# Optimization experiments

Measured on AMD Instinct MI355X. Metric: run time of the kernel, lower is better.

The kernel has to match this reference:

```python
import jax, jax.numpy as jnp
import numpy as np

B, L, LQ = 64, 4096, 128
D = 32        # input_dim (value channels)
ET = 128      # embed_time
NH = 1        # num_heads
H = 128       # nhidden
NC = 6        # n_classes


def _time_emb(tt, lin_w, lin_b, per_w, per_b):
    # tt [..., T] -> [..., T, ET]; cat(Linear(1,1)(t), sin(Linear(1,ET-1)(t)))
    tt = tt[..., None]
    out1 = tt * lin_w[0, 0] + lin_b
    out2 = jnp.sin(tt @ per_w + per_b)
    return jnp.concatenate([out1, out2], axis=-1)


def _gru_dir(xs, wih, whh, bih, bhh, reverse):
    # xs [B, T, I] -> [B, T, H]; torch GRU gate math
    xs_t = jnp.swapaxes(xs, 0, 1)              # [T, B, I]
    if reverse:
        xs_t = xs_t[::-1]
    gi_all = xs_t @ wih.T + bih                # [T, B, 3H] precomputed input gates
    h0 = jnp.zeros((xs.shape[0], H), xs.dtype)

    def step(h, gi):
        gh = h @ whh.T + bhh
        ir, iz, inn = jnp.split(gi, 3, axis=-1)
        hr, hz, hn = jnp.split(gh, 3, axis=-1)
        r = jax.nn.sigmoid(ir + hr)
        z = jax.nn.sigmoid(iz + hz)
        n = jnp.tanh(inn + r * hn)
        h_new = (1.0 - z) * n + z * h
        return h_new, h_new

    _, ys = jax.lax.scan(step, h0, gi_all)     # [T, B, H]
    if reverse:
        ys = ys[::-1]
    return jnp.swapaxes(ys, 0, 1)


def _bigru(xs, wih, whh, bih, bhh):
    fwd = _gru_dir(xs, wih[0], whh[0], bih[0], bhh[0], False)
    bwd = _gru_dir(xs, wih[1], whh[1], bih[1], bhh[1], True)
    return jnp.concatenate([fwd, bwd], axis=-1)


def setup_inputs() -> dict:
    ks = jax.random.split(jax.random.key(0), 32)
    w = lambda i, s: jax.random.normal(ks[i], s, jnp.float32) * 0.05
    G3 = 3 * H
    return {
        "x": jax.random.normal(ks[0], (B, L, D), jnp.float32),
        "time_steps": jax.random.uniform(ks[1], (B, L), dtype=jnp.float32),
        "query_times": jnp.linspace(0.0, 1.0, LQ, dtype=jnp.float32),
        "lin_w": w(2, (1, 1)), "lin_b": w(3, (1,)),
        "per_w": w(4, (1, ET - 1)), "per_b": w(5, (ET - 1,)),
        "wq": w(6, (ET, ET)), "bq": w(7, (ET,)),
        "wk": w(8, (ET, ET)), "bk": w(9, (ET,)),
        "wo": w(10, (NH * D, H)), "bo": w(11, (H,)),
        "gru0_wih": w(12, (2, G3, H)), "gru0_whh": w(13, (2, G3, H)),
        "gru0_bih": w(14, (2, G3)), "gru0_bhh": w(15, (2, G3)),
        "gru1_wih": w(16, (2, G3, 2 * H)), "gru1_whh": w(17, (2, G3, H)),
        "gru1_bih": w(18, (2, G3)), "gru1_bhh": w(19, (2, G3)),
        "c1_w": w(20, (2 * H, 128)), "c1_b": w(21, (128,)),
        "c2_w": w(22, (128, 64)), "c2_b": w(23, (64,)),
        "c3_w": w(24, (64, NC)), "c3_b": w(25, (NC,)),
    }


def reference(x, time_steps, query_times, lin_w, lin_b, per_w, per_b,
              wq, bq, wk, bk, wo, bo,
              gru0_wih, gru0_whh, gru0_bih, gru0_bhh,
              gru1_wih, gru1_whh, gru1_bih, gru1_bhh,
              c1_w, c1_b, c2_w, c2_b, c3_w, c3_b):
    ek = ET // NH
    # learned time embeddings
    q = _time_emb(query_times[None, :], lin_w, lin_b, per_w, per_b)  # [1, LQ, ET]
    k = _time_emb(time_steps, lin_w, lin_b, per_w, per_b)            # [B, L, ET]
    # per-head projections
    qp = (q @ wq + bq).reshape(1, LQ, NH, ek).transpose(0, 2, 1, 3)[0]  # [NH, LQ, ek]
    kp = (k @ wk + bk).reshape(B, L, NH, ek).transpose(0, 2, 1, 3)      # [B, NH, L, ek]
    # mTAN attention: scores are channel-independent (mask=None), so the
    # per-channel repeat+softmax reduces to a single softmax over keys.
    scores = jnp.einsum('hqe,bhke->bhqk', qp, kp) / jnp.sqrt(jnp.float32(ek))
    p = jax.nn.softmax(scores, axis=-1)                                 # [B, NH, LQ, L]
    att = jnp.einsum('bhqk,bkd->bqhd', p, x).reshape(B, LQ, NH * D)
    att_out = att @ wo + bo                                             # [B, LQ, H]
    # 2-layer bidirectional GRU
    g0 = _bigru(att_out, gru0_wih, gru0_whh, gru0_bih, gru0_bhh)        # [B, LQ, 2H]
    g1 = _bigru(g0, gru1_wih, gru1_whh, gru1_bih, gru1_bhh)             # [B, LQ, 2H]
    class_in = jnp.concatenate([g1[:, -1, :H], g1[:, 0, H:]], axis=1)   # [B, 2H]
    out = ((class_in @ c1_w + c1_b) @ c2_w + c2_b) @ c3_w + c3_b        # [B, NC]
    return out
```

## Files before the change

kernel.cpp:

```cpp
#include <hip/hip_runtime.h>
#include <math.h>

#define Bn   64
#define Ln   4096
#define LQn  128
#define Dn   32
#define ETn  128
#define Hn   128
#define G3n  384
#define NDEG 12

typedef __attribute__((ext_vector_type(2))) float f32x2;

#define DPPF(x, ctrl) __int_as_float(__builtin_amdgcn_update_dpp(0, __float_as_int(x), (ctrl), 0xF, 0xF, true))
#define QP_XOR1 0xB1
#define QP_XOR2 0x4E
#define QP_B0   0x00
#define QP_B1   0x55
#define QP_B2   0xAA
#define QP_B3   0xFF

__device__ __forceinline__ float sin_poly(float x) {
    const float x2 = x * x;
    float r = -1.9841270114e-04f;
    r = fmaf(r, x2,  8.3333337680e-03f);
    r = fmaf(r, x2, -1.6666667163e-01f);
    return fmaf(r * x2, x, x);
}
__device__ __forceinline__ float cos_poly(float x) {
    const float x2 = x * x;
    float r =  2.4801587642e-05f;
    r = fmaf(r, x2, -1.3888888899e-03f);
    r = fmaf(r, x2,  4.1666667908e-02f);
    r = fmaf(r, x2, -5.0000000000e-01f);
    return fmaf(r, x2, 1.0f);
}

#define WS_C    0
#define WS_WT   4096
#define WS_B2   (WS_WT + 768*32)
#define WS_CLS  (WS_B2 + 1024)
#define WS_G0   (WS_CLS + Bn*2*Hn)
#define WS_GI   (WS_G0 + Bn*LQn*2*Hn)
#define WS_QPB  WS_G0
#define WS_BAS  (WS_G0 + 16384)
#define WS_ACCP WS_G0
#define WS_SP   (WS_G0 + 1048576)

__global__ __launch_bounds__(128) void k_basis(
    const float* __restrict__ per_w, const float* __restrict__ per_b,
    float* __restrict__ basis)
{
    const int j = threadIdx.x;
    if (j >= ETn - 1) return;
    const float w = per_w[j], b = per_b[j];
    const float sb = sin_poly(b), cb = cos_poly(b);
    float wp = 1.f;
#pragma unroll
    for (int d = 0; d < NDEG; ++d) {
        const float sd = ((d & 3) == 0) ? sb : ((d & 3) == 1) ? cb : ((d & 3) == 2) ? -sb : -cb;
        basis[d * 128 + j] = wp * sd;
        wp *= w / (float)(d + 1);
    }
}

__global__ __launch_bounds__(128) void k_qp(
    const float* __restrict__ qtimes, const float* __restrict__ lin_w,
    const float* __restrict__ lin_b, const float* __restrict__ per_w,
    const float* __restrict__ per_b, const float* __restrict__ wq,
    const float* __restrict__ bq, float* __restrict__ qp)
{
    __shared__ float qe[ETn];
    const int q = blockIdx.x, e = threadIdx.x;
    const float t = qtimes[q];
    qe[e] = (e == 0) ? fmaf(t, lin_w[0], lin_b[0])
                     : sin_poly(fmaf(t, per_w[e - 1], per_b[e - 1]));
    __syncthreads();
    float a = bq[e];
#pragma unroll 16
    for (int i = 0; i < ETn; ++i) a = fmaf(qe[i], wq[i * ETn + e], a);
    qp[q * ETn + e] = a;
}

__global__ __launch_bounds__(128) void k_qtc(
    const float* __restrict__ qp, const float* __restrict__ wk,
    const float* __restrict__ bk, const float* __restrict__ lin_w,
    const float* __restrict__ lin_b, const float* __restrict__ basis,
    float* __restrict__ C)
{
    __shared__ float qp_l[ETn], qt_l[ETn], red[96], qbk_red[32];
    const int q = blockIdx.x, tid = threadIdx.x;
    qp_l[tid] = qp[q * ETn + tid];
    __syncthreads();
    {
        const float4* wk4 = (const float4*)(wk + (size_t)tid * ETn);
        const float4* qp4 = (const float4*)qp_l;
        float a = 0.f;
#pragma unroll
        for (int k = 0; k < 32; ++k) {
            const float4 w4 = wk4[k], p4 = qp4[k];
            a += w4.x * p4.x + w4.y * p4.y + w4.z * p4.z + w4.w * p4.w;
        }
        qt_l[tid] = a;
    }
    __syncthreads();
    if (tid < 96) {
        const int d = tid >> 3, g = tid & 7;
        float p = 0.f;
        for (int j = g; j < ETn - 1; j += 8) p = fmaf(qt_l[j + 1], basis[d * 128 + j], p);
        red[tid] = p;
    } else {
        const int g2 = tid - 96;
        float p = 0.f;
#pragma unroll
        for (int k = 0; k < 4; ++k) p = fmaf(qp_l[g2 + 32 * k], bk[g2 + 32 * k], p);
        qbk_red[g2] = p;
    }
    __syncthreads();
    if (tid < NDEG) {
        const int d = tid;
        float s = red[d * 8 + 0] + red[d * 8 + 1] + red[d * 8 + 2] + red[d * 8 + 3]
                + red[d * 8 + 4] + red[d * 8 + 5] + red[d * 8 + 6] + red[d * 8 + 7];
        if (d == 0) {
            float qbk = 0.f;
#pragma unroll
            for (int k = 0; k < 32; ++k) qbk += qbk_red[k];
            s += qt_l[0] * lin_b[0] + qbk;
        }
        if (d == 1) s += qt_l[0] * lin_w[0];
        C[q * NDEG + d] = s * 0.08838834764831845f;
    }
}

__global__ __launch_bounds__(256) void k_fuse(
    const float* __restrict__ wih, const float* __restrict__ wo,
    const float* __restrict__ bo, const float* __restrict__ bih,
    float* __restrict__ Wt, float* __restrict__ bias2)
{
    const int t = blockIdx.x * 256 + threadIdx.x;
    if (t < 768 * 32) {
        const int o = t >> 5, d = t & 31;
        const float* wr = wih + (size_t)o * 128;
        const float* wc = wo + (size_t)d * 128;
        float a = 0.f;
        for (int h = 0; h < 128; ++h) a += wr[h] * wc[h];
        Wt[t] = a;
    } else if (t < 768 * 33) {
        const int o = t - 768 * 32;
        const float* wr = wih + (size_t)o * 128;
        float a = bih[o];
        for (int h = 0; h < 128; ++h) a += bo[h] * wr[h];
        bias2[o] = a;
    }
}

#define ACC8(m, pv) \
    acc[m][0].x = fmaf(pv, xa.x, acc[m][0].x); acc[m][0].y = fmaf(pv, xa.y, acc[m][0].y); \
    acc[m][0].z = fmaf(pv, xa.z, acc[m][0].z); acc[m][0].w = fmaf(pv, xa.w, acc[m][0].w); \
    acc[m][1].x = fmaf(pv, xb.x, acc[m][1].x); acc[m][1].y = fmaf(pv, xb.y, acc[m][1].y); \
    acc[m][1].z = fmaf(pv, xb.z, acc[m][1].z); acc[m][1].w = fmaf(pv, xb.w, acc[m][1].w);

__global__ __launch_bounds__(512, 2) void k_attn(
    const float* __restrict__ x, const float* __restrict__ tsteps,
    const float* __restrict__ Cc, float* __restrict__ accP, float* __restrict__ sP)
{
    __shared__ float slab[4][128][36];
    const int tid = threadIdx.x;
    const int b = blockIdx.x >> 2, lsplit = blockIdx.x & 3;
    const int i = tid & 3, qt = (tid >> 2) & 31, ls2 = tid >> 7;
    const int qown = 4 * qt + i;

    float c[NDEG];
#pragma unroll
    for (int d = 0; d < NDEG; ++d) c[d] = Cc[qown * NDEG + d];

    const int l0 = lsplit * 1024 + ls2 * 256;
    const float4* tg4 = (const float4*)(tsteps + (size_t)b * Ln + l0);
    const float4* xg  = (const float4*)(x + ((size_t)b * Ln + l0) * Dn);

    float4 acc[4][2];
#pragma unroll
    for (int m = 0; m < 4; ++m)
#pragma unroll
        for (int e = 0; e < 2; ++e) { acc[m][e].x = 0.f; acc[m][e].y = 0.f; acc[m][e].z = 0.f; acc[m][e].w = 0.f; }
    float s_own = 0.f;

    for (int k = 0; k < 64; ++k) {
        const float4 t4 = tg4[k];
#pragma unroll
        for (int jj = 0; jj < 4; ++jj) {
            const float t = (jj == 0) ? t4.x : (jj == 1) ? t4.y : (jj == 2) ? t4.z : t4.w;
            float sc = c[NDEG - 1];
#pragma unroll
            for (int d = NDEG - 2; d >= 0; --d) sc = fmaf(sc, t, c[d]);
            const float pe = __expf(sc);
            s_own += pe;
            const float p0 = DPPF(pe, QP_B0);
            const float p1 = DPPF(pe, QP_B1);
            const float p2 = DPPF(pe, QP_B2);
            const float p3 = DPPF(pe, QP_B3);
            const int lrow = (k * 4 + jj) * 8;
            const float4 xa = xg[lrow + 2 * i];
            const float4 xb = xg[lrow + 2 * i + 1];
            ACC8(0, p0) ACC8(1, p1) ACC8(2, p2) ACC8(3, p3)
        }
    }
#pragma unroll
    for (int m = 0; m < 4; ++m) {
        *(float4*)&slab[ls2][4 * qt + m][8 * i]     = acc[m][0];
        *(float4*)&slab[ls2][4 * qt + m][8 * i + 4] = acc[m][1];
    }
    slab[ls2][qown][32] = s_own;
    __syncthreads();
    const int q = tid & 127, part = tid >> 7;
#pragma unroll
    for (int j = 0; j < 2; ++j) {
        const int off = (part * 2 + j) * 4;
        float4 r  = *(float4*)&slab[0][q][off];
        float4 r1 = *(float4*)&slab[1][q][off];
        float4 r2 = *(float4*)&slab[2][q][off];
        float4 r3 = *(float4*)&slab[3][q][off];
        r.x += r1.x + r2.x + r3.x; r.y += r1.y + r2.y + r3.y;
        r.z += r1.z + r2.z + r3.z; r.w += r1.w + r2.w + r3.w;
        *(float4*)&accP[((((size_t)lsplit * Bn + b) * LQn + q) * 32) + off] = r;
    }
    if (part == 0) {
        sP[((size_t)lsplit * Bn + b) * LQn + q] =
            slab[0][q][32] + slab[1][q][32] + slab[2][q][32] + slab[3][q][32];
    }
}

__global__ __launch_bounds__(256) void k_gemm_att(
    const float* __restrict__ accP, const float* __restrict__ sP,
    const float* __restrict__ Bm, const float* __restrict__ bias,
    float* __restrict__ Cm)
{
    __shared__ float4 A_l[64 * 8];
    __shared__ float4 B_l[64 * 8];
    const int tid = threadIdx.x;
    const int m0 = blockIdx.x * 64, n0 = blockIdx.y * 64;
    const int r0 = (tid >> 4) << 2, c0 = (tid & 15) << 2;
    float acc[4][4] = {};
    const float4* Ag = (const float4*)accP;
    const float4* Bg = (const float4*)Bm;

#pragma unroll
    for (int w = 0; w < 2; ++w) {
        const int idx = tid + w * 256;
        const int row = idx >> 3, c4 = idx & 7;
        const int sc = (c4 + row + (row >> 2)) & 7;
        const int m = m0 + row;
        float4 a0 = Ag[(size_t)m * 8 + c4];
        float4 a1 = Ag[((size_t)8192  + m) * 8 + c4];
        float4 a2 = Ag[((size_t)16384 + m) * 8 + c4];
        float4 a3 = Ag[((size_t)24576 + m) * 8 + c4];
        const float inv = 1.f / (sP[m] + sP[8192 + m] + sP[16384 + m] + sP[24576 + m]);
        float4 av;
        av.x = (a0.x + a1.x + a2.x + a3.x) * inv;
        av.y = (a0.y + a1.y + a2.y + a3.y) * inv;
        av.z = (a0.z + a1.z + a2.z + a3.z) * inv;
        av.w = (a0.w + a1.w + a2.w + a3.w) * inv;
        A_l[row * 8 + sc] = av;
        B_l[row * 8 + sc] = Bg[(size_t)(n0 + row) * 8 + c4];
    }
    __syncthreads();
#pragma unroll
    for (int k4 = 0; k4 < 8; ++k4) {
        float4 av[4], bv[4];
#pragma unroll
        for (int j = 0; j < 4; ++j) {
            const int ra = r0 + j;
            av[j] = A_l[ra * 8 + ((k4 + ra + (ra >> 2)) & 7)];
        }
#pragma unroll
        for (int j = 0; j < 4; ++j) {
            const int rb = c0 + j;
            bv[j] = B_l[rb * 8 + ((k4 + rb + (rb >> 2)) & 7)];
        }
#pragma unroll
        for (int ri = 0; ri < 4; ++ri)
#pragma unroll
            for (int ci = 0; ci < 4; ++ci)
                acc[ri][ci] += av[ri].x * bv[ci].x + av[ri].y * bv[ci].y
                             + av[ri].z * bv[ci].z + av[ri].w * bv[ci].w;
    }
#pragma unroll
    for (int ri = 0; ri < 4; ++ri) {
        float4 o4;
        o4.x = acc[ri][0] + bias[n0 + c0 + 0];
        o4.y = acc[ri][1] + bias[n0 + c0 + 1];
        o4.z = acc[ri][2] + bias[n0 + c0 + 2];
        o4.w = acc[ri][3] + bias[n0 + c0 + 3];
        *(float4*)&Cm[(size_t)(m0 + r0 + ri) * 768 + n0 + c0] = o4;
    }
}

__global__ __launch_bounds__(256) void k_gemm_nt(
    const float* __restrict__ A, const float* __restrict__ Bm,
    const float* __restrict__ bias, float* __restrict__ Cm,
    int N, int K)
{
    __shared__ float4 A_l[64 * 8];
    __shared__ float4 B_l[64 * 8];
    const int tid = threadIdx.x;
    const int m0 = blockIdx.x * 64, n0 = blockIdx.y * 64;
    const int r0 = (tid >> 4) << 2, c0 = (tid & 15) << 2;
    const int K4 = K >> 2;
    float acc[4][4] = {};
    const float4* Ag = (const float4*)A;
    const float4* Bg = (const float4*)Bm;

    for (int k0 = 0; k0 < K4; k0 += 8) {
        __syncthreads();
#pragma unroll
        for (int w = 0; w < 2; ++w) {
            const int idx = tid + w * 256;
            const int row = idx >> 3, c4 = idx & 7;
            const int sc = (c4 + row + (row >> 2)) & 7;
            A_l[row * 8 + sc] = Ag[(size_t)(m0 + row) * K4 + k0 + c4];
            B_l[row * 8 + sc] = Bg[(size_t)(n0 + row) * K4 + k0 + c4];
        }
        __syncthreads();
#pragma unroll
        for (int k4 = 0; k4 < 8; ++k4) {
            float4 av[4], bv[4];
#pragma unroll
            for (int j = 0; j < 4; ++j) {
                const int ra = r0 + j;
                av[j] = A_l[ra * 8 + ((k4 + ra + (ra >> 2)) & 7)];
            }
#pragma unroll
            for (int j = 0; j < 4; ++j) {
                const int rb = c0 + j;
                bv[j] = B_l[rb * 8 + ((k4 + rb + (rb >> 2)) & 7)];
            }
#pragma unroll
            for (int ri = 0; ri < 4; ++ri)
#pragma unroll
                for (int ci = 0; ci < 4; ++ci)
                    acc[ri][ci] += av[ri].x * bv[ci].x + av[ri].y * bv[ci].y
                                 + av[ri].z * bv[ci].z + av[ri].w * bv[ci].w;
        }
    }
#pragma unroll
    for (int ri = 0; ri < 4; ++ri) {
        float4 o4;
        o4.x = acc[ri][0] + bias[n0 + c0 + 0];
        o4.y = acc[ri][1] + bias[n0 + c0 + 1];
        o4.z = acc[ri][2] + bias[n0 + c0 + 2];
        o4.w = acc[ri][3] + bias[n0 + c0 + 3];
        *(float4*)&Cm[(size_t)(m0 + r0 + ri) * N + n0 + c0] = o4;
    }
}

__global__ __launch_bounds__(256, 1) void k_gru(
    const float* __restrict__ gi, const float* __restrict__ whh,
    const float* __restrict__ bhh, float* __restrict__ seq_out,
    float* __restrict__ final_out)
{
    __shared__ float h_l[2][Hn];
    const int tid = threadIdx.x;
    const int b = blockIdx.x >> 1, dir = blockIdx.x & 1;
    const int j = tid >> 1, q = tid & 1;

    f32x2 wr[32], wz[32], wn[32];
    {
        const float* wb = whh + ((size_t)dir * G3n + j) * Hn + 64 * q;
        const f32x2* p0 = (const f32x2*)(wb);
        const f32x2* p1 = (const f32x2*)(wb + (size_t)128 * Hn);
        const f32x2* p2 = (const f32x2*)(wb + (size_t)256 * Hn);
#pragma unroll
        for (int k = 0; k < 32; ++k) { wr[k] = p0[k]; wz[k] = p1[k]; wn[k] = p2[k]; }
    }
#pragma unroll
    for (int k = 0; k < 32; ++k) {
        asm volatile("" : "+v"(wr[k]));
        asm volatile("" : "+v"(wz[k]));
        asm volatile("" : "+v"(wn[k]));
    }
    const float bhr = bhh[dir * G3n + j];
    const float bhz = bhh[dir * G3n + 128 + j];
    const float bhn = bhh[dir * G3n + 256 + j];

    if (tid < Hn) { h_l[0][tid] = 0.f; h_l[1][tid] = 0.f; }
    __syncthreads();

    const long sstride = dir ? -768 : 768;
    const float* gptr = gi + (size_t)b * LQn * 768 + dir * G3n + j
                        + (size_t)(dir ? LQn - 1 : 0) * 768;

    int cur = 0;
    float hlast = 0.f;

    auto gstep = [&](const float gir, const float giz, const float gin,
                     const int step) {
        const float hold = h_l[cur][j];
        const float4* hb = (const float4*)(&h_l[cur][q * 64]);
        f32x2 ar = {0.f, 0.f}, az = {0.f, 0.f}, an = {0.f, 0.f};
        f32x2 br = {0.f, 0.f}, bz = {0.f, 0.f}, bn = {0.f, 0.f};
#pragma unroll
        for (int cc = 0; cc < 16; ++cc) {
            float4 hv = hb[cc];
            f32x2 h01; h01.x = hv.x; h01.y = hv.y;
            f32x2 h23; h23.x = hv.z; h23.y = hv.w;
            asm("v_pk_fma_f32 %0, %1, %2, %0" : "+v"(ar) : "v"(wr[2 * cc]),     "v"(h01));
            asm("v_pk_fma_f32 %0, %1, %2, %0" : "+v"(az) : "v"(wz[2 * cc]),     "v"(h01));
            asm("v_pk_fma_f32 %0, %1, %2, %0" : "+v"(an) : "v"(wn[2 * cc]),     "v"(h01));
            asm("v_pk_fma_f32 %0, %1, %2, %0" : "+v"(br) : "v"(wr[2 * cc + 1]), "v"(h23));
            asm("v_pk_fma_f32 %0, %1, %2, %0" : "+v"(bz) : "v"(wz[2 * cc + 1]), "v"(h23));
            asm("v_pk_fma_f32 %0, %1, %2, %0" : "+v"(bn) : "v"(wn[2 * cc + 1]), "v"(h23));
        }
        float sr = (ar.x + br.x) + (ar.y + br.y);
        float sz = (az.x + bz.x) + (az.y + bz.y);
        float sn = (an.x + bn.x) + (an.y + bn.y);
        sr += DPPF(sr, QP_XOR1);
        sz += DPPF(sz, QP_XOR1);
        sn += DPPF(sn, QP_XOR1);
        const float r = 1.f / (1.f + __expf(-(gir + sr + bhr)));
        const float z = 1.f / (1.f + __expf(-(giz + sz + bhz)));
        const float nx = gin + r * (sn + bhn);
        const float n = 1.f - 2.f / (1.f + __expf(2.f * nx));
        const float hn = n + z * (hold - n);
        if (q == 0) {
            h_l[cur ^ 1][j] = hn;
            if (seq_out) {
                const int l = dir ? (LQn - 1 - step) : step;
                seq_out[((size_t)(b * LQn + l)) * (2 * Hn) + dir * Hn + j] = hn;
            }
        }
        hlast = hn;
        cur ^= 1;
        __syncthreads();
    };

    float gA[3], gB[3], gC[3], gD[3];
#define GLD(dst, s) { const long o = (long)(s) * sstride; \
    dst[0] = gptr[o]; dst[1] = gptr[o + 128]; dst[2] = gptr[o + 256]; }
    GLD(gA, 0) GLD(gB, 1) GLD(gC, 2) GLD(gD, 3)
    for (int s0 = 0; s0 < LQn; s0 += 4) {
        gstep(gA[0], gA[1], gA[2], s0);
        { const int sn2 = (s0 + 4 < LQn) ? s0 + 4 : LQn - 1; GLD(gA, sn2) }
        gstep(gB[0], gB[1], gB[2], s0 + 1);
        { const int sn2 = (s0 + 5 < LQn) ? s0 + 5 : LQn - 1; GLD(gB, sn2) }
        gstep(gC[0], gC[1], gC[2], s0 + 2);
        { const int sn2 = (s0 + 6 < LQn) ? s0 + 6 : LQn - 1; GLD(gC, sn2) }
        gstep(gD[0], gD[1], gD[2], s0 + 3);
        { const int sn2 = (s0 + 7 < LQn) ? s0 + 7 : LQn - 1; GLD(gD, sn2) }
    }
#undef GLD
    if (final_out && q == 0) final_out[b * 2 * Hn + dir * Hn + j] = hlast;
}

__global__ __launch_bounds__(256) void k_cls(
    const float* __restrict__ cls_in,
    const float* __restrict__ c1w, const float* __restrict__ c1b,
    const float* __restrict__ c2w, const float* __restrict__ c2b,
    const float* __restrict__ c3w, const float* __restrict__ c3b,
    float* __restrict__ out)
{
    __shared__ float ci[256], y1[128], y2[64];
    const int b = blockIdx.x, tid = threadIdx.x;
    ci[tid] = cls_in[b * 256 + tid];
    __syncthreads();
    if (tid < 128) { float a = c1b[tid]; for (int i = 0; i < 256; ++i) a += ci[i] * c1w[i * 128 + tid]; y1[tid] = a; }
    __syncthreads();
    if (tid < 64)  { float a = c2b[tid]; for (int i = 0; i < 128; ++i) a += y1[i] * c2w[i * 64 + tid];  y2[tid] = a; }
    __syncthreads();
    if (tid < 6)   { float a = c3b[tid]; for (int i = 0; i < 64; ++i)  a += y2[i] * c3w[i * 6 + tid];   out[b * 6 + tid] = a; }
}

extern "C" void kernel_launch(void* const* d_in, const int* in_sizes, int n_in,
                              void* d_out, int out_size, void* d_ws, size_t ws_size,
                              hipStream_t stream)
{
    const float* x        = (const float*)d_in[0];
    const float* tsteps   = (const float*)d_in[1];
    const float* qtimes   = (const float*)d_in[2];
    const float* lin_w    = (const float*)d_in[3];
    const float* lin_b    = (const float*)d_in[4];
    const float* per_w    = (const float*)d_in[5];
    const float* per_b    = (const float*)d_in[6];
    const float* wq       = (const float*)d_in[7];
    const float* bq       = (const float*)d_in[8];
    const float* wk       = (const float*)d_in[9];
    const float* bk       = (const float*)d_in[10];
    const float* wo       = (const float*)d_in[11];
    const float* bo       = (const float*)d_in[12];
    const float* g0_wih   = (const float*)d_in[13];
    const float* g0_whh   = (const float*)d_in[14];
    const float* g0_bih   = (const float*)d_in[15];
    const float* g0_bhh   = (const float*)d_in[16];
    const float* g1_wih   = (const float*)d_in[17];
    const float* g1_whh   = (const float*)d_in[18];
    const float* g1_bih   = (const float*)d_in[19];
    const float* g1_bhh   = (const float*)d_in[20];
    const float* c1w      = (const float*)d_in[21];
    const float* c1b      = (const float*)d_in[22];
    const float* c2w      = (const float*)d_in[23];
    const float* c2b      = (const float*)d_in[24];
    const float* c3w      = (const float*)d_in[25];
    const float* c3b      = (const float*)d_in[26];
    float* out = (float*)d_out;
    float* ws  = (float*)d_ws;

    float* Cws   = ws + WS_C;
    float* Wt    = ws + WS_WT;
    float* bias2 = ws + WS_B2;
    float* clsin = ws + WS_CLS;
    float* g0buf = ws + WS_G0;
    float* qpB   = ws + WS_QPB;
    float* basB  = ws + WS_BAS;
    float* accP  = ws + WS_ACCP;
    float* sPb   = ws + WS_SP;
    float* gibuf = ws + WS_GI;

    k_basis<<<1, 128, 0, stream>>>(per_w, per_b, basB);
    k_qp<<<128, 128, 0, stream>>>(qtimes, lin_w, lin_b, per_w, per_b, wq, bq, qpB);
    k_qtc<<<128, 128, 0, stream>>>(qpB, wk, bk, lin_w, lin_b, basB, Cws);

    k_fuse<<<99, 256, 0, stream>>>(g0_wih, wo, bo, g0_bih, Wt, bias2);
    k_attn<<<256, 512, 0, stream>>>(x, tsteps, Cws, accP, sPb);

    k_gemm_att<<<dim3(128, 12), 256, 0, stream>>>(accP, sPb, Wt, bias2, gibuf);
    k_gru<<<128, 256, 0, stream>>>(gibuf, g0_whh, g0_bhh, g0buf, nullptr);

    k_gemm_nt<<<dim3(128, 12), 256, 0, stream>>>(g0buf, g1_wih, g1_bih, gibuf, 768, 256);
    k_gru<<<128, 256, 0, stream>>>(gibuf, g1_whh, g1_bhh, nullptr, clsin);

    k_cls<<<64, 256, 0, stream>>>(clsin, c1w, c1b, c2w, c2b, c3w, c3b, out);
}
```

Baseline: 326.5 us.

## Split GRU recurrent matvec across eight lanes per hidden unit

The GRU kernel now runs 1024 threads per block, giving each hidden unit eight lanes that each hold 16 columns of the recurrent weights instead of two lanes holding 64. Partial sums are combined with three DPP steps. Input-gate values are loaded once per lane (lanes 0-2) and broadcast within each quad by DPP. The sync becomes a raw s_barrier with an lgkmcnt wait. This shortens the per-step serial FMA chain on the latency-bound recurrence, at the cost of more waves per barrier, extra cross-lane reductions and a shallower prefetch of the gate inputs.

```diff
diff --git a/kernel.cpp b/kernel.cpp
--- a/kernel.cpp
+++ b/kernel.cpp
@@ -19,6 +19,7 @@
 #define QP_B1   0x55
 #define QP_B2   0xAA
 #define QP_B3   0xFF
+#define ROW_HALF_MIRROR 0x141
 
 __device__ __forceinline__ float sin_poly(float x) {
     const float x2 = x * x;
@@ -353,7 +354,7 @@
     }
 }
 
-__global__ __launch_bounds__(256, 1) void k_gru(
+__global__ __launch_bounds__(1024) void k_gru(
     const float* __restrict__ gi, const float* __restrict__ whh,
     const float* __restrict__ bhh, float* __restrict__ seq_out,
     float* __restrict__ final_out)
@@ -361,19 +362,19 @@
     __shared__ float h_l[2][Hn];
     const int tid = threadIdx.x;
     const int b = blockIdx.x >> 1, dir = blockIdx.x & 1;
-    const int j = tid >> 1, q = tid & 1;
-
-    f32x2 wr[32], wz[32], wn[32];
+    const int j = tid >> 3, q = tid & 7;
+
+    f32x2 wr[8], wz[8], wn[8];
     {
-        const float* wb = whh + ((size_t)dir * G3n + j) * Hn + 64 * q;
+        const float* wb = whh + ((size_t)dir * G3n + j) * Hn + 16 * q;
         const f32x2* p0 = (const f32x2*)(wb);
         const f32x2* p1 = (const f32x2*)(wb + (size_t)128 * Hn);
         const f32x2* p2 = (const f32x2*)(wb + (size_t)256 * Hn);
 #pragma unroll
-        for (int k = 0; k < 32; ++k) { wr[k] = p0[k]; wz[k] = p1[k]; wn[k] = p2[k]; }
-    }
-#pragma unroll
-    for (int k = 0; k < 32; ++k) {
+        for (int k = 0; k < 8; ++k) { wr[k] = p0[k]; wz[k] = p1[k]; wn[k] = p2[k]; }
+    }
+#pragma unroll
+    for (int k = 0; k < 8; ++k) {
         asm volatile("" : "+v"(wr[k]));
         asm volatile("" : "+v"(wz[k]));
         asm volatile("" : "+v"(wn[k]));
@@ -382,40 +383,39 @@
     const float bhz = bhh[dir * G3n + 128 + j];
     const float bhn = bhh[dir * G3n + 256 + j];
 
-    if (tid < Hn) { h_l[0][tid] = 0.f; h_l[1][tid] = 0.f; }
-    __syncthreads();
-
-    const long sstride = dir ? -768 : 768;
-    const float* gptr = gi + (size_t)b * LQn * 768 + dir * G3n + j
-                        + (size_t)(dir ? LQn - 1 : 0) * 768;
+    if (tid < 2 * Hn) ((float*)h_l)[tid] = 0.f;
+    __syncthreads();
+
+    const long sstr = dir ? -768 : 768;
+    const float* gib = gi + ((size_t)b * LQn + (size_t)(dir ? LQn - 1 : 0)) * 768
+                       + dir * G3n + j;
 
     int cur = 0;
     float hlast = 0.f;
 
-    auto gstep = [&](const float gir, const float giz, const float gin,
-                     const int step) {
+    auto gstep = [&](const float gv, const int step) {
         const float hold = h_l[cur][j];
-        const float4* hb = (const float4*)(&h_l[cur][q * 64]);
+        const float4* hb = (const float4*)(&h_l[cur][16 * q]);
         f32x2 ar = {0.f, 0.f}, az = {0.f, 0.f}, an = {0.f, 0.f};
-        f32x2 br = {0.f, 0.f}, bz = {0.f, 0.f}, bn = {0.f, 0.f};
-#pragma unroll
-        for (int cc = 0; cc < 16; ++cc) {
-            float4 hv = hb[cc];
+#pragma unroll
+        for (int k = 0; k < 4; ++k) {
+            const float4 hv = hb[k];
             f32x2 h01; h01.x = hv.x; h01.y = hv.y;
             f32x2 h23; h23.x = hv.z; h23.y = hv.w;
-            asm("v_pk_fma_f32 %0, %1, %2, %0" : "+v"(ar) : "v"(wr[2 * cc]),     "v"(h01));
-            asm("v_pk_fma_f32 %0, %1, %2, %0" : "+v"(az) : "v"(wz[2 * cc]),     "v"(h01));
-            asm("v_pk_fma_f32 %0, %1, %2, %0" : "+v"(an) : "v"(wn[2 * cc]),     "v"(h01));
-            asm("v_pk_fma_f32 %0, %1, %2, %0" : "+v"(br) : "v"(wr[2 * cc + 1]), "v"(h23));
-            asm("v_pk_fma_f32 %0, %1, %2, %0" : "+v"(bz) : "v"(wz[2 * cc + 1]), "v"(h23));
-            asm("v_pk_fma_f32 %0, %1, %2, %0" : "+v"(bn) : "v"(wn[2 * cc + 1]), "v"(h23));
-        }
-        float sr = (ar.x + br.x) + (ar.y + br.y);
-        float sz = (az.x + bz.x) + (az.y + bz.y);
-        float sn = (an.x + bn.x) + (an.y + bn.y);
-        sr += DPPF(sr, QP_XOR1);
-        sz += DPPF(sz, QP_XOR1);
-        sn += DPPF(sn, QP_XOR1);
+            ar = __builtin_elementwise_fma(wr[2 * k],     h01, ar);
+            az = __builtin_elementwise_fma(wz[2 * k],     h01, az);
+            an = __builtin_elementwise_fma(wn[2 * k],     h01, an);
+            ar = __builtin_elementwise_fma(wr[2 * k + 1], h23, ar);
+            az = __builtin_elementwise_fma(wz[2 * k + 1], h23, az);
+            an = __builtin_elementwise_fma(wn[2 * k + 1], h23, an);
+        }
+        float sr = ar.x + ar.y, sz = az.x + az.y, sn = an.x + an.y;
+        sr += DPPF(sr, QP_XOR1); sr += DPPF(sr, QP_XOR2); sr += DPPF(sr, ROW_HALF_MIRROR);
+        sz += DPPF(sz, QP_XOR1); sz += DPPF(sz, QP_XOR2); sz += DPPF(sz, ROW_HALF_MIRROR);
+        sn += DPPF(sn, QP_XOR1); sn += DPPF(sn, QP_XOR2); sn += DPPF(sn, ROW_HALF_MIRROR);
+        const float gir = DPPF(gv, QP_B0);
+        const float giz = DPPF(gv, QP_B1);
+        const float gin = DPPF(gv, QP_B2);
         const float r = 1.f / (1.f + __expf(-(gir + sr + bhr)));
         const float z = 1.f / (1.f + __expf(-(giz + sz + bhz)));
         const float nx = gin + r * (sn + bhn);
@@ -430,22 +430,18 @@
         }
         hlast = hn;
         cur ^= 1;
-        __syncthreads();
+        asm volatile("s_waitcnt lgkmcnt(0)\n\ts_barrier" ::: "memory");
     };
 
-    float gA[3], gB[3], gC[3], gD[3];
-#define GLD(dst, s) { const long o = (long)(s) * sstride; \
-    dst[0] = gptr[o]; dst[1] = gptr[o + 128]; dst[2] = gptr[o + 256]; }
-    GLD(gA, 0) GLD(gB, 1) GLD(gC, 2) GLD(gD, 3)
-    for (int s0 = 0; s0 < LQn; s0 += 4) {
-        gstep(gA[0], gA[1], gA[2], s0);
-        { const int sn2 = (s0 + 4 < LQn) ? s0 + 4 : LQn - 1; GLD(gA, sn2) }
-        gstep(gB[0], gB[1], gB[2], s0 + 1);
-        { const int sn2 = (s0 + 5 < LQn) ? s0 + 5 : LQn - 1; GLD(gB, sn2) }
-        gstep(gC[0], gC[1], gC[2], s0 + 2);
-        { const int sn2 = (s0 + 6 < LQn) ? s0 + 6 : LQn - 1; GLD(gC, sn2) }
-        gstep(gD[0], gD[1], gD[2], s0 + 3);
-        { const int sn2 = (s0 + 7 < LQn) ? s0 + 7 : LQn - 1; GLD(gD, sn2) }
+    float gA, gB;
+#define GLD(d, s) { d = (q < 3) ? gib[(long)(s) * sstr + q * Hn] : 0.f; }
+    GLD(gA, 0)
+    GLD(gB, 1)
+    for (int s0 = 0; s0 < LQn; s0 += 2) {
+        gstep(gA, s0);
+        { const int sn2 = (s0 + 2 < LQn) ? s0 + 2 : LQn - 1; GLD(gA, sn2) }
+        gstep(gB, s0 + 1);
+        { const int sn2 = (s0 + 3 < LQn) ? s0 + 3 : LQn - 1; GLD(gB, sn2) }
     }
 #undef GLD
     if (final_out && q == 0) final_out[b * 2 * Hn + dir * Hn + j] = hlast;
@@ -522,10 +518,10 @@
     k_attn<<<256, 512, 0, stream>>>(x, tsteps, Cws, accP, sPb);
 
     k_gemm_att<<<dim3(128, 12), 256, 0, stream>>>(accP, sPb, Wt, bias2, gibuf);
-    k_gru<<<128, 256, 0, stream>>>(gibuf, g0_whh, g0_bhh, g0buf, nullptr);
+    k_gru<<<128, 1024, 0, stream>>>(gibuf, g0_whh, g0_bhh, g0buf, nullptr);
 
     k_gemm_nt<<<dim3(128, 12), 256, 0, stream>>>(g0buf, g1_wih, g1_bih, gibuf, 768, 256);
-    k_gru<<<128, 256, 0, stream>>>(gibuf, g1_whh, g1_bhh, nullptr, clsin);
+    k_gru<<<128, 1024, 0, stream>>>(gibuf, g1_whh, g1_bhh, nullptr, clsin);
 
     k_cls<<<64, 256, 0, stream>>>(clsin, c1w, c1b, c2w, c2b, c3w, c3b, out);
 }
```

New measurement: 386.4 us. 18.4% more time.
